# Kernel tuning notes

Hardware: AMD Instinct MI355X
Metric: run time of the kernel (lower is better)

## Reference

```python
import jax, jax.numpy as jnp
import numpy as np
from jax import lax

EPS = 1e-5
K = 20

def _bn_lrelu(h, g, b, m, v):
    # inference-style BatchNorm (channel-last) + LeakyReLU(0.2)
    h = (h - m) * (g * lax.rsqrt(v + EPS)) + b
    return jnp.where(h > 0, h, 0.2 * h)

def _edgeconv(x, W, g, b, m, v):
    # x: (B, N, C) -> (B, N, O)
    xx = jnp.sum(x * x, axis=-1)
    # negative squared pairwise distance: -||xi||^2 - ||xj||^2 + 2 xi.xj
    d = 2.0 * jnp.einsum('bnc,bmc->bnm', x, x) - xx[:, :, None] - xx[:, None, :]
    idx = lax.top_k(d, K)[1]  # (B, N, K) indices of nearest neighbors (incl. self)
    nbr = jax.vmap(lambda xb, ib: xb[ib])(x, idx)  # (B, N, K, C)
    ctr = x[:, :, None, :]
    edge = jnp.concatenate([jnp.broadcast_to(ctr, nbr.shape), nbr - ctr], axis=-1)  # (B,N,K,2C)
    h = jnp.einsum('bnkc,oc->bnko', edge, W)  # 1x1 Conv2d, no bias
    h = _bn_lrelu(h, g, b, m, v)
    return jnp.max(h, axis=2)  # max over K neighbors -> (B, N, O)

def _forward(pts, w1, g1, b1, m1, v1, w2, g2, b2, m2, v2, w3, g3, b3, m3, v3, w4, g4, b4, m4, v4, wg, gg, bg, mg, vg):
    x1 = _edgeconv(pts, w1, g1, b1, m1, v1)   # (B,N,64)
    x2 = _edgeconv(x1, w2, g2, b2, m2, v2)    # (B,N,64)
    x3 = _edgeconv(x2, w3, g3, b3, m3, v3)    # (B,N,128)
    x4 = _edgeconv(x3, w4, g4, b4, m4, v4)    # (B,N,256)
    xcat = jnp.concatenate([x1, x2, x3, x4], axis=-1)  # (B,N,512)
    h = jnp.einsum('bnc,oc->bno', xcat, wg)   # 1x1 Conv1d, no bias
    h = _bn_lrelu(h, gg, bg, mg, vg)
    return jnp.max(h, axis=1)[:, :, None]     # (B, feat_dims, 1)

def setup_inputs():
    key = jax.random.key(0)
    ks = jax.random.split(key, 8)
    B, N = 8, 2048
    def w(k_, o, i):
        return jax.random.normal(k_, (o, i), jnp.float32) / np.float32(np.sqrt(i))
    def bn(k_, c):
        k1, k2, k3, k4 = jax.random.split(k_, 4)
        return (jax.random.uniform(k1, (c,), jnp.float32, 0.5, 1.5),
                jax.random.normal(k2, (c,), jnp.float32) * 0.1,
                jax.random.normal(k3, (c,), jnp.float32) * 0.1,
                jax.random.uniform(k4, (c,), jnp.float32, 0.5, 1.5))
    inp = {'pts': jax.random.normal(ks[0], (B, N, 3), jnp.float32)}
    chans = [(3, 64), (64, 64), (64, 128), (128, 256)]
    for i, (ci, co) in enumerate(chans, start=1):
        inp[f'w{i}'] = w(jax.random.fold_in(ks[1], i), co, 2 * ci)
        g, b, m, v = bn(jax.random.fold_in(ks[2], i), co)
        inp[f'g{i}'], inp[f'b{i}'], inp[f'm{i}'], inp[f'v{i}'] = g, b, m, v
    inp['wg'] = w(ks[3], 512, 512)
    inp['gg'], inp['bg'], inp['mg'], inp['vg'] = bn(ks[4], 512)
    return inp

def reference(pts, w1, g1, b1, m1, v1, w2, g2, b2, m2, v2, w3, g3, b3, m3, v3, w4, g4, b4, m4, v4, wg, gg, bg, mg, vg):
    return _forward(pts, w1, g1, b1, m1, v1, w2, g2, b2, m2, v2, w3, g3, b3, m3, v3, w4, g4, b4, m4, v4, wg, gg, bg, mg, vg)
```

## Files before the change

kernel.cpp:

```cpp
#include <hip/hip_runtime.h>
#include <hip/hip_bf16.h>

#define EPS 1e-5f

typedef __attribute__((ext_vector_type(8))) short bf16x8;
typedef __attribute__((ext_vector_type(4))) float f32x4;

__device__ __forceinline__ unsigned int fkey(float f) {
    unsigned int b = __float_as_uint(f);
    return (b & 0x80000000u) ? ~b : (b | 0x80000000u);
}
__device__ __forceinline__ float funkey(unsigned int k) {
    unsigned int b = (k & 0x80000000u) ? (k & 0x7fffffffu) : ~k;
    return __uint_as_float(b);
}
__device__ __forceinline__ unsigned short f2bu(float f) {
    union { __hip_bfloat16 h; unsigned short u; } cv;
    cv.h = __float2bfloat16(f);
    return cv.u;
}
__device__ __forceinline__ float bu2f(unsigned short u) {
    return __uint_as_float(((unsigned int)u) << 16);
}
__device__ __forceinline__ void hilo(float v, unsigned short& h, unsigned short& l) {
    h = f2bu(v);
    l = f2bu(v - bu2f(h));
}

__global__ void wfrag_kernel(const float* __restrict__ W, int CO, int C2, int C2P,
                             unsigned short* __restrict__ Fh, unsigned short* __restrict__ Fl) {
    int id = blockIdx.x * 256 + threadIdx.x;
    int total = CO * C2P;
    if (id >= total) return;
    int j = id & 7, lane = (id >> 3) & 63, t = id >> 9;
    int KS = C2P >> 5;
    int ks = t % KS, ot = t / KS;
    int o = ot * 16 + (lane & 15);
    int c = ks * 32 + ((lane >> 4) << 3) + j;
    float v = (c < C2) ? W[o * C2 + c] : 0.f;
    unsigned short h, l;
    hilo(v, h, l);
    Fh[id] = h;
    Fl[id] = l;
}

__global__ void xfrag_kernel(const float* __restrict__ feat, int fs, int C, int KS,
                             unsigned short* __restrict__ Fh, unsigned short* __restrict__ Fl) {
    const int N = 2048, NT = 128;
    int id = blockIdx.x * 256 + threadIdx.x;
    int total = 8 * NT * KS * 512;
    if (id >= total) return;
    int j = id & 7, lane = (id >> 3) & 63;
    int rest = id >> 9;
    int ks = rest % KS;
    int bt = rest / KS;
    int t = bt & 127, b = bt >> 7;
    int row = t * 16 + (lane & 15);
    int c = ks * 32 + ((lane >> 4) << 3) + j;
    float v = (c < C) ? feat[((size_t)(b * N + row)) * fs + c] : 0.f;
    unsigned short h, l;
    hilo(v, h, l);
    Fh[id] = h;
    Fl[id] = l;
}

__global__ void sumsq_feat_kernel(const float* __restrict__ feat, int fs, int C,
                                  float* __restrict__ xx) {
    int id = blockIdx.x * 256 + threadIdx.x;
    if (id >= 8 * 2048) return;
    const float* p = feat + (size_t)id * fs;
    float s = 0.f;
    if ((C & 3) == 0) {
        for (int c = 0; c < C; c += 4) {
            float4 v = *(const float4*)(p + c);
            s = fmaf(v.x, v.x, s); s = fmaf(v.y, v.y, s);
            s = fmaf(v.z, v.z, s); s = fmaf(v.w, v.w, s);
        }
    } else {
        for (int c = 0; c < C; ++c) { float v = p[c]; s = fmaf(v, v, s); }
    }
    xx[id] = s;
}

template <int CP>
__global__ __launch_bounds__(512, 4) void
dist_topk_mfma(const unsigned short* __restrict__ Fh, const unsigned short* __restrict__ Fl,
               const float* __restrict__ xx, int* __restrict__ idxOut) {
    const int N = 2048, NT = 128, CAP = 448;
    constexpr int KS = CP / 32;
    int b  = blockIdx.x & 7;
    int mt = blockIdx.x >> 3;
    int tid = threadIdx.x, lane = tid & 63, wv = tid >> 6;

    __shared__ unsigned int gmax[16][64];
    __shared__ unsigned int Tsh[16];
    __shared__ unsigned int cnt[16];
    __shared__ unsigned long long cand[16][CAP];

    bf16x8 Ah[KS], Al[KS];
#pragma unroll
    for (int ks = 0; ks < KS; ++ks) {
        size_t fi = (((size_t)(b * NT + mt) * KS + ks) << 9) + (lane << 3);
        Ah[ks] = *(const bf16x8*)(Fh + fi);
        Al[ks] = *(const bf16x8*)(Fl + fi);
    }
    int rbase = (lane >> 4) << 2;
    float xxr[4];
#pragma unroll
    for (int rr = 0; rr < 4; ++rr) xxr[rr] = xx[b * N + mt * 16 + rbase + rr];

    auto gramkeys = [&](int ct, unsigned int* kout) {
        f32x4 acc;
#pragma unroll
        for (int rr = 0; rr < 4; ++rr) acc[rr] = 0.f;
#pragma unroll
        for (int ks = 0; ks < KS; ++ks) {
            size_t fi = (((size_t)(b * NT + ct) * KS + ks) << 9) + (lane << 3);
            bf16x8 Bh = *(const bf16x8*)(Fh + fi);
            bf16x8 Bl = *(const bf16x8*)(Fl + fi);
            acc = __builtin_amdgcn_mfma_f32_16x16x32_bf16(Al[ks], Bh, acc, 0, 0, 0);
            acc = __builtin_amdgcn_mfma_f32_16x16x32_bf16(Ah[ks], Bl, acc, 0, 0, 0);
            acc = __builtin_amdgcn_mfma_f32_16x16x32_bf16(Ah[ks], Bh, acc, 0, 0, 0);
        }
        float xxm = xx[b * N + ct * 16 + (lane & 15)];
#pragma unroll
        for (int rr = 0; rr < 4; ++rr)
            kout[rr] = fkey(2.f * acc[rr] - xxr[rr] - xxm);
    };

    unsigned int rmax0[4], rmax1[4];
#pragma unroll
    for (int rr = 0; rr < 4; ++rr) { rmax0[rr] = 0u; rmax1[rr] = 0u; }

    for (int i = 0; i < 8; ++i) {
        unsigned int kk[4];
        gramkeys(wv * 16 + i, kk);
#pragma unroll
        for (int rr = 0; rr < 4; ++rr) rmax0[rr] = rmax0[rr] > kk[rr] ? rmax0[rr] : kk[rr];
    }
    for (int i = 8; i < 16; ++i) {
        unsigned int kk[4];
        gramkeys(wv * 16 + i, kk);
#pragma unroll
        for (int rr = 0; rr < 4; ++rr) rmax1[rr] = rmax1[rr] > kk[rr] ? rmax1[rr] : kk[rr];
    }
#pragma unroll
    for (int s = 4; s <= 8; s <<= 1)
#pragma unroll
        for (int rr = 0; rr < 4; ++rr) {
            unsigned int o0 = (unsigned int)__shfl_xor((int)rmax0[rr], s);
            rmax0[rr] = rmax0[rr] > o0 ? rmax0[rr] : o0;
            unsigned int o1 = (unsigned int)__shfl_xor((int)rmax1[rr], s);
            rmax1[rr] = rmax1[rr] > o1 ? rmax1[rr] : o1;
        }
    if ((lane & 15) < 4) {
#pragma unroll
        for (int rr = 0; rr < 4; ++rr) {
            gmax[rbase + rr][wv * 8 + (lane & 3)]     = rmax0[rr];
            gmax[rbase + rr][wv * 8 + 4 + (lane & 3)] = rmax1[rr];
        }
    }
    __syncthreads();

#pragma unroll
    for (int pass = 0; pass < 2; ++pass) {
        int row = wv + 8 * pass;
        unsigned int S = gmax[row][lane];
#pragma unroll
        for (int k = 2; k <= 64; k <<= 1)
#pragma unroll
            for (int j2 = k >> 1; j2 > 0; j2 >>= 1) {
                unsigned int o = (unsigned int)__shfl_xor((int)S, j2);
                bool keepMax = (((lane & j2) == 0) == ((lane & k) == 0));
                unsigned int mx = S > o ? S : o;
                unsigned int mn = S > o ? o : S;
                S = keepMax ? mx : mn;
            }
        if (lane == 19) Tsh[row] = S;
        if (lane == 0) cnt[row] = 0u;
    }
    __syncthreads();

    for (int i = 0; i < 16; ++i) {
        int ct = wv * 16 + i;
        unsigned int kk[4];
        gramkeys(ct, kk);
        int m = ct * 16 + (lane & 15);
#pragma unroll
        for (int rr = 0; rr < 4; ++rr) {
            int row = rbase + rr;
            if (kk[rr] >= Tsh[row]) {
                unsigned int slot = atomicAdd(&cnt[row], 1u);
                if (slot < CAP)
                    cand[row][slot] = ((unsigned long long)kk[rr] << 16) |
                                      (unsigned long long)(0xFFFFu - (unsigned int)m);
            }
        }
    }
    __syncthreads();

#pragma unroll
    for (int pass = 0; pass < 2; ++pass) {
        int row = wv + 8 * pass;
        unsigned int nc = cnt[row];
        if (nc <= 64u) {
            unsigned long long P = (lane < (int)nc) ? cand[row][lane] : 0ULL;
#pragma unroll
            for (int k = 2; k <= 64; k <<= 1)
#pragma unroll
                for (int j2 = k >> 1; j2 > 0; j2 >>= 1) {
                    unsigned long long o = __shfl_xor(P, j2);
                    bool keepMax = (((lane & j2) == 0) == ((lane & k) == 0));
                    unsigned long long mx = P > o ? P : o;
                    unsigned long long mn = P > o ? o : P;
                    P = keepMax ? mx : mn;
                }
            if (lane < 20)
                idxOut[((size_t)b * N + mt * 16 + row) * 20 + lane] =
                    (int)(0xFFFFu - (unsigned int)(P & 0xFFFFu));
        } else {
            unsigned int ncc = nc < CAP ? nc : CAP;
            unsigned long long P0 = ((unsigned int)(lane)       < ncc) ? cand[row][lane]       : 0ULL;
            unsigned long long P1 = ((unsigned int)(lane + 64)  < ncc) ? cand[row][lane + 64]  : 0ULL;
            unsigned long long P2 = ((unsigned int)(lane + 128) < ncc) ? cand[row][lane + 128] : 0ULL;
            unsigned long long P3 = ((unsigned int)(lane + 192) < ncc) ? cand[row][lane + 192] : 0ULL;
            unsigned long long P4 = ((unsigned int)(lane + 256) < ncc) ? cand[row][lane + 256] : 0ULL;
            unsigned long long P5 = ((unsigned int)(lane + 320) < ncc) ? cand[row][lane + 320] : 0ULL;
            unsigned long long P6 = ((unsigned int)(lane + 384) < ncc) ? cand[row][lane + 384] : 0ULL;
            int resm = 0;
            for (int k = 0; k < 20; ++k) {
                unsigned long long lmx = P0;
                lmx = lmx > P1 ? lmx : P1;
                lmx = lmx > P2 ? lmx : P2;
                lmx = lmx > P3 ? lmx : P3;
                lmx = lmx > P4 ? lmx : P4;
                lmx = lmx > P5 ? lmx : P5;
                lmx = lmx > P6 ? lmx : P6;
#pragma unroll
                for (int s = 1; s < 64; s <<= 1) {
                    unsigned long long o = __shfl_xor(lmx, s);
                    lmx = lmx > o ? lmx : o;
                }
                P0 = (P0 == lmx) ? 0ULL : P0;
                P1 = (P1 == lmx) ? 0ULL : P1;
                P2 = (P2 == lmx) ? 0ULL : P2;
                P3 = (P3 == lmx) ? 0ULL : P3;
                P4 = (P4 == lmx) ? 0ULL : P4;
                P5 = (P5 == lmx) ? 0ULL : P5;
                P6 = (P6 == lmx) ? 0ULL : P6;
                if (lane == k) resm = (int)(0xFFFFu - (unsigned int)(lmx & 0xFFFFu));
            }
            if (lane < 20) idxOut[((size_t)b * N + mt * 16 + row) * 20 + lane] = resm;
        }
    }
}

template <int CI, int CO, int TN, int WAVES, int NKC>
__global__ __launch_bounds__(WAVES * 64) void
edgeconv_mfma(const float* __restrict__ feat, int fs, const int* __restrict__ idx,
              const unsigned short* __restrict__ Wh, const unsigned short* __restrict__ Wl,
              const float* __restrict__ gp, const float* __restrict__ bp,
              const float* __restrict__ mp, const float* __restrict__ vp,
              float* __restrict__ outBase) {
    constexpr int N = 2048, K = 20;
    constexpr int C2 = 2 * CI;
    constexpr int C2P = (C2 < 32) ? 32 : C2;
    constexpr int KS = C2P / 32;
    constexpr int KSC = KS / NKC;
    constexpr int CCOLS = KSC * 32;
    constexpr int CHB = CCOLS * 2;
    constexpr int OT = CO / 16;
    constexpr int OTW = OT / WAVES;
    constexpr int M = TN * K;
    constexpr int MT = M / 16;
    constexpr int CH = CCOLS / 8;
    constexpr int SWZ = (CHB >= 128) ? 7 : (CHB / 16 - 1);
    constexpr int THREADS = WAVES * 64;

    int b  = blockIdx.x & 7;
    int n0 = (blockIdx.x >> 3) * TN;
    int tid = threadIdx.x;
    int lane = tid & 63, wv = tid >> 6;

    __shared__ float ctr[TN][CI];
    __shared__ int nb[M];
    __shared__ __align__(16) unsigned char Eh[M * CHB];
    __shared__ __align__(16) unsigned char El[M * CHB];

    for (int e = tid; e < TN * CI; e += THREADS) {
        int ln = e / CI, c = e % CI;
        ctr[ln][c] = feat[((size_t)b * N + n0 + ln) * fs + c];
    }
    for (int e = tid; e < M; e += THREADS) {
        int k = e / TN, ln = e % TN;
        nb[e] = idx[((size_t)b * N + n0 + ln) * K + k];
    }
    __syncthreads();

    f32x4 acc[MT][OTW];
#pragma unroll
    for (int mt = 0; mt < MT; ++mt)
#pragma unroll
        for (int ot = 0; ot < OTW; ++ot)
#pragma unroll
            for (int rr = 0; rr < 4; ++rr) acc[mt][ot][rr] = 0.f;

    for (int kc = 0; kc < NKC; ++kc) {
        if (kc) __syncthreads();
        for (int e = tid; e < M * CH; e += THREADS) {
            int mrow = e / CH, ch = e - mrow * CH;
            int c0 = kc * CCOLS + ch * 8;
            int ln = mrow % TN;
            float v[8];
            if constexpr (CI >= 8) {
                if (c0 < CI) {
#pragma unroll
                    for (int j = 0; j < 8; ++j) v[j] = ctr[ln][c0 + j];
                } else {
                    int c1 = c0 - CI;
                    const float* nrow = feat + ((size_t)b * N + nb[mrow]) * fs + c1;
                    float4 a  = *(const float4*)nrow;
                    float4 b4 = *(const float4*)(nrow + 4);
                    v[0] = a.x  - ctr[ln][c1 + 0];
                    v[1] = a.y  - ctr[ln][c1 + 1];
                    v[2] = a.z  - ctr[ln][c1 + 2];
                    v[3] = a.w  - ctr[ln][c1 + 3];
                    v[4] = b4.x - ctr[ln][c1 + 4];
                    v[5] = b4.y - ctr[ln][c1 + 5];
                    v[6] = b4.z - ctr[ln][c1 + 6];
                    v[7] = b4.w - ctr[ln][c1 + 7];
                }
            } else {
                if (c0 == 0) {
                    const float* nrow = feat + ((size_t)b * N + nb[mrow]) * fs;
                    v[0] = ctr[ln][0]; v[1] = ctr[ln][1]; v[2] = ctr[ln][2];
                    v[3] = nrow[0] - ctr[ln][0];
                    v[4] = nrow[1] - ctr[ln][1];
                    v[5] = nrow[2] - ctr[ln][2];
                    v[6] = 0.f; v[7] = 0.f;
                } else {
#pragma unroll
                    for (int j = 0; j < 8; ++j) v[j] = 0.f;
                }
            }
            union { unsigned short u[8]; uint4 v4; } th, tl;
#pragma unroll
            for (int j = 0; j < 8; ++j) hilo(v[j], th.u[j], tl.u[j]);
            int off = mrow * CHB + ((ch * 16) ^ ((mrow & SWZ) << 4));
            *(uint4*)&Eh[off] = th.v4;
            *(uint4*)&El[off] = tl.v4;
        }
        __syncthreads();

        bf16x8 Bh[OTW][KSC], Bl[OTW][KSC];
#pragma unroll
        for (int ot = 0; ot < OTW; ++ot)
#pragma unroll
            for (int ksc = 0; ksc < KSC; ++ksc) {
                size_t fi = (size_t)((((wv * OTW + ot) * KS + kc * KSC + ksc) * 64 + lane)) << 3;
                Bh[ot][ksc] = *(const bf16x8*)(Wh + fi);
                Bl[ot][ksc] = *(const bf16x8*)(Wl + fi);
            }

#pragma unroll
        for (int mt = 0; mt < MT; ++mt) {
            int r0 = mt * 16 + (lane & 15);
            int cb = (lane >> 4) << 4;
            bf16x8 Ah[KSC], Al[KSC];
#pragma unroll
            for (int ksc = 0; ksc < KSC; ++ksc) {
                int off = r0 * CHB + (((ksc << 6) + cb) ^ ((r0 & SWZ) << 4));
                Ah[ksc] = *(const bf16x8*)&Eh[off];
                Al[ksc] = *(const bf16x8*)&El[off];
            }
#pragma unroll
            for (int ksc = 0; ksc < KSC; ++ksc)
#pragma unroll
                for (int ot = 0; ot < OTW; ++ot) {
                    acc[mt][ot] = __builtin_amdgcn_mfma_f32_16x16x32_bf16(Al[ksc], Bh[ot][ksc], acc[mt][ot], 0, 0, 0);
                    acc[mt][ot] = __builtin_amdgcn_mfma_f32_16x16x32_bf16(Ah[ksc], Bl[ot][ksc], acc[mt][ot], 0, 0, 0);
                    acc[mt][ot] = __builtin_amdgcn_mfma_f32_16x16x32_bf16(Ah[ksc], Bh[ot][ksc], acc[mt][ot], 0, 0, 0);
                }
        }
    }

#pragma unroll
    for (int ot = 0; ot < OTW; ++ot) {
        f32x4 v;
#pragma unroll
        for (int rr = 0; rr < 4; ++rr) {
            float m = acc[0][ot][rr];
#pragma unroll
            for (int mt = 1; mt < MT; ++mt) m = fmaxf(m, acc[mt][ot][rr]);
            if constexpr (TN == 4) m = fmaxf(m, __shfl_xor(m, 16));
            m = fmaxf(m, __shfl_xor(m, 32));
            v[rr] = m;
        }
        int o = (wv * OTW + ot) * 16 + (lane & 15);
        float s  = gp[o] * rsqrtf(vp[o] + EPS);
        float sh = bp[o] - mp[o] * s;
        bool valid = (TN == 8) ? (lane < 32) : (lane < 16);
        if (valid) {
            int lnb = (TN == 8) ? ((lane >> 4) << 2) : 0;
#pragma unroll
            for (int rr = 0; rr < 4; ++rr) {
                float h = fmaf(v[rr], s, sh);
                h = h > 0.f ? h : 0.2f * h;
                outBase[((size_t)b * N + n0 + lnb + rr) * 512 + o] = h;
            }
        }
    }
}

__global__ __launch_bounds__(256) void
global_mfma(const float* __restrict__ xcat,
            const unsigned short* __restrict__ Wh, const unsigned short* __restrict__ Wl,
            const float* __restrict__ gg, const float* __restrict__ bg,
            const float* __restrict__ mg, const float* __restrict__ vg,
            unsigned int* __restrict__ keys) {
    const int N = 2048, CV = 512;
    int b     = blockIdx.x & 7;
    int t     = blockIdx.x >> 3;
    int n0    = (t & 63) * 32;
    int colh  = t >> 6;
    int tid = threadIdx.x, lane = tid & 63, wv = tid >> 6;
    int obase = colh * 16 + wv * 4;

    f32x4 acc0[4], acc1[4];
#pragma unroll
    for (int ot = 0; ot < 4; ++ot)
#pragma unroll
        for (int rr = 0; rr < 4; ++rr) { acc0[ot][rr] = 0.f; acc1[ot][rr] = 0.f; }

    const float* arow0 = xcat + ((size_t)b * N + n0 +      (lane & 15)) * CV + ((lane >> 4) << 3);
    const float* arow1 = xcat + ((size_t)b * N + n0 + 16 + (lane & 15)) * CV + ((lane >> 4) << 3);

    for (int ks = 0; ks < 16; ++ks) {
        bf16x8 Ah0, Al0, Ah1, Al1;
        {
            float4 a  = *(const float4*)(arow0 + ks * 32);
            float4 b4 = *(const float4*)(arow0 + ks * 32 + 4);
            union { unsigned short u[8]; bf16x8 v; } ch, cl;
            hilo(a.x,  ch.u[0], cl.u[0]); hilo(a.y,  ch.u[1], cl.u[1]);
            hilo(a.z,  ch.u[2], cl.u[2]); hilo(a.w,  ch.u[3], cl.u[3]);
            hilo(b4.x, ch.u[4], cl.u[4]); hilo(b4.y, ch.u[5], cl.u[5]);
            hilo(b4.z, ch.u[6], cl.u[6]); hilo(b4.w, ch.u[7], cl.u[7]);
            Ah0 = ch.v; Al0 = cl.v;
        }
        {
            float4 a  = *(const float4*)(arow1 + ks * 32);
            float4 b4 = *(const float4*)(arow1 + ks * 32 + 4);
            union { unsigned short u[8]; bf16x8 v; } ch, cl;
            hilo(a.x,  ch.u[0], cl.u[0]); hilo(a.y,  ch.u[1], cl.u[1]);
            hilo(a.z,  ch.u[2], cl.u[2]); hilo(a.w,  ch.u[3], cl.u[3]);
            hilo(b4.x, ch.u[4], cl.u[4]); hilo(b4.y, ch.u[5], cl.u[5]);
            hilo(b4.z, ch.u[6], cl.u[6]); hilo(b4.w, ch.u[7], cl.u[7]);
            Ah1 = ch.v; Al1 = cl.v;
        }
#pragma unroll
        for (int ot = 0; ot < 4; ++ot) {
            size_t fi = (size_t)((((obase + ot) * 16 + ks) * 64 + lane)) << 3;
            bf16x8 Bh = *(const bf16x8*)(Wh + fi);
            bf16x8 Bl = *(const bf16x8*)(Wl + fi);
            acc0[ot] = __builtin_amdgcn_mfma_f32_16x16x32_bf16(Al0, Bh, acc0[ot], 0, 0, 0);
            acc0[ot] = __builtin_amdgcn_mfma_f32_16x16x32_bf16(Ah0, Bl, acc0[ot], 0, 0, 0);
            acc0[ot] = __builtin_amdgcn_mfma_f32_16x16x32_bf16(Ah0, Bh, acc0[ot], 0, 0, 0);
            acc1[ot] = __builtin_amdgcn_mfma_f32_16x16x32_bf16(Al1, Bh, acc1[ot], 0, 0, 0);
            acc1[ot] = __builtin_amdgcn_mfma_f32_16x16x32_bf16(Ah1, Bl, acc1[ot], 0, 0, 0);
            acc1[ot] = __builtin_amdgcn_mfma_f32_16x16x32_bf16(Ah1, Bh, acc1[ot], 0, 0, 0);
        }
    }

#pragma unroll
    for (int ot = 0; ot < 4; ++ot) {
        f32x4 v;
#pragma unroll
        for (int rr = 0; rr < 4; ++rr) {
            float m = fmaxf(acc0[ot][rr], acc1[ot][rr]);
            m = fmaxf(m, __shfl_xor(m, 16));
            m = fmaxf(m, __shfl_xor(m, 32));
            v[rr] = m;
        }
        int o = (obase + ot) * 16 + (lane & 15);
        float s  = gg[o] * rsqrtf(vg[o] + EPS);
        float sh = bg[o] - mg[o] * s;
        if (lane < 16) {
            float hm = -INFINITY;
#pragma unroll
            for (int rr = 0; rr < 4; ++rr) {
                float h = fmaf(v[rr], s, sh);
                h = h > 0.f ? h : 0.2f * h;
                hm = fmaxf(hm, h);
            }
            atomicMax(&keys[b * 512 + o], fkey(hm));
        }
    }
}

__global__ void decode_kernel(const unsigned int* __restrict__ keys, float* __restrict__ out) {
    int id = blockIdx.x * 256 + threadIdx.x;
    if (id < 8 * 512) out[id] = funkey(keys[id]);
}

extern "C" void kernel_launch(void* const* d_in, const int* in_sizes, int n_in,
                              void* d_out, int out_size, void* d_ws, size_t ws_size,
                              hipStream_t stream) {
    const int B = 8, N = 2048, K = 20;
    const float* pts = (const float*)d_in[0];
    const float* w1 = (const float*)d_in[1];
    const float *g1 = (const float*)d_in[2], *b1 = (const float*)d_in[3],
                *m1 = (const float*)d_in[4], *v1 = (const float*)d_in[5];
    const float* w2 = (const float*)d_in[6];
    const float *g2 = (const float*)d_in[7], *b2 = (const float*)d_in[8],
                *m2 = (const float*)d_in[9], *v2 = (const float*)d_in[10];
    const float* w3 = (const float*)d_in[11];
    const float *g3 = (const float*)d_in[12], *b3 = (const float*)d_in[13],
                *m3 = (const float*)d_in[14], *v3 = (const float*)d_in[15];
    const float* w4 = (const float*)d_in[16];
    const float *g4 = (const float*)d_in[17], *b4 = (const float*)d_in[18],
                *m4 = (const float*)d_in[19], *v4 = (const float*)d_in[20];
    const float* wg = (const float*)d_in[21];
    const float *gg = (const float*)d_in[22], *bg = (const float*)d_in[23],
                *mg = (const float*)d_in[24], *vg = (const float*)d_in[25];

    float* ws   = (float*)d_ws;
    float* xcat = ws;
    float* xx   = xcat + (size_t)B * N * 512;
    int*   idx  = (int*)(xx + B * N);
    unsigned short* Fdh = (unsigned short*)(idx + (size_t)B * N * K);
    unsigned short* Fdl = Fdh + (size_t)B * N * 128;
    unsigned short* wf1h = Fdl + (size_t)B * N * 128;
    unsigned short* wf1l = wf1h + 64 * 32;
    unsigned short* wf2h = wf1l + 64 * 32;
    unsigned short* wf2l = wf2h + 64 * 128;
    unsigned short* wf3h = wf2l + 64 * 128;
    unsigned short* wf3l = wf3h + 128 * 128;
    unsigned short* wf4h = wf3l + 128 * 128;
    unsigned short* wf4l = wf4h + 256 * 256;
    unsigned short* wfgh = wf4l + 256 * 256;
    unsigned short* wfgl = wfgh + 512 * 512;
    unsigned int* keys  = (unsigned int*)(wfgl + 512 * 512);

    wfrag_kernel<<<(64 * 32 + 255) / 256, 256, 0, stream>>>(w1, 64, 6, 32, wf1h, wf1l);
    wfrag_kernel<<<(64 * 128 + 255) / 256, 256, 0, stream>>>(w2, 64, 128, 128, wf2h, wf2l);
    wfrag_kernel<<<(128 * 128 + 255) / 256, 256, 0, stream>>>(w3, 128, 128, 128, wf3h, wf3l);
    wfrag_kernel<<<(256 * 256 + 255) / 256, 256, 0, stream>>>(w4, 256, 256, 256, wf4h, wf4l);
    wfrag_kernel<<<(512 * 512 + 255) / 256, 256, 0, stream>>>(wg, 512, 512, 512, wfgh, wfgl);

    xfrag_kernel<<<(8 * 128 * 1 * 512 + 255) / 256, 256, 0, stream>>>(pts, 3, 3, 1, Fdh, Fdl);
    sumsq_feat_kernel<<<(B * N + 255) / 256, 256, 0, stream>>>(pts, 3, 3, xx);
    dist_topk_mfma<32><<<B * (N / 16), 512, 0, stream>>>(Fdh, Fdl, xx, idx);
    edgeconv_mfma<3, 64, 8, 4, 1><<<B * (N / 8), 256, 0, stream>>>(pts, 3, idx, wf1h, wf1l, g1, b1, m1, v1, xcat + 0);

    xfrag_kernel<<<(8 * 128 * 2 * 512 + 255) / 256, 256, 0, stream>>>(xcat + 0, 512, 64, 2, Fdh, Fdl);
    sumsq_feat_kernel<<<(B * N + 255) / 256, 256, 0, stream>>>(xcat + 0, 512, 64, xx);
    dist_topk_mfma<64><<<B * (N / 16), 512, 0, stream>>>(Fdh, Fdl, xx, idx);
    edgeconv_mfma<64, 64, 4, 4, 1><<<B * (N / 4), 256, 0, stream>>>(xcat + 0, 512, idx, wf2h, wf2l, g2, b2, m2, v2, xcat + 64);

    xfrag_kernel<<<(8 * 128 * 2 * 512 + 255) / 256, 256, 0, stream>>>(xcat + 64, 512, 64, 2, Fdh, Fdl);
    sumsq_feat_kernel<<<(B * N + 255) / 256, 256, 0, stream>>>(xcat + 64, 512, 64, xx);
    dist_topk_mfma<64><<<B * (N / 16), 512, 0, stream>>>(Fdh, Fdl, xx, idx);
    edgeconv_mfma<64, 128, 4, 8, 1><<<B * (N / 4), 512, 0, stream>>>(xcat + 64, 512, idx, wf3h, wf3l, g3, b3, m3, v3, xcat + 128);

    xfrag_kernel<<<(8 * 128 * 4 * 512 + 255) / 256, 256, 0, stream>>>(xcat + 128, 512, 128, 4, Fdh, Fdl);
    sumsq_feat_kernel<<<(B * N + 255) / 256, 256, 0, stream>>>(xcat + 128, 512, 128, xx);
    dist_topk_mfma<128><<<B * (N / 16), 512, 0, stream>>>(Fdh, Fdl, xx, idx);
    edgeconv_mfma<128, 256, 4, 8, 2><<<B * (N / 4), 512, 0, stream>>>(xcat + 128, 512, idx, wf4h, wf4l, g4, b4, m4, v4, xcat + 256);

    hipMemsetAsync(keys, 0, (size_t)B * 512 * sizeof(unsigned int), stream);
    global_mfma<<<B * 128, 256, 0, stream>>>(xcat, wfgh, wfgl, gg, bg, mg, vg, keys);
    decode_kernel<<<(B * 512 + 255) / 256, 256, 0, stream>>>(keys, (float*)d_out);
}
```

Baseline: 506.2 us.

## Split edge conv weights into center and difference parts, precompute center term per point

Splits each EdgeConv weight into a center half and a neighbor-difference half. The center contribution W_c·x_i is computed once per point by a new ctr_mfma kernel that reuses the existing distance fragments, rather than once for each of the K neighbors. The edge kernel then multiplies only the difference features and adds the precomputed center term before BN and LeakyReLU, which halves its GEMM K dimension and its LDS staging and removes the multi-chunk loop. In exchange it adds one kernel launch per layer and a global buffer write and read for the center outputs.

```diff
diff --git a/kernel.cpp b/kernel.cpp
--- a/kernel.cpp
+++ b/kernel.cpp
@@ -27,7 +27,7 @@
     l = f2bu(v - bu2f(h));
 }
 
-__global__ void wfrag_kernel(const float* __restrict__ W, int CO, int C2, int C2P,
+__global__ void wfrag_kernel(const float* __restrict__ W, int CO, int CIN, int coff, int CW, int C2P,
                              unsigned short* __restrict__ Fh, unsigned short* __restrict__ Fl) {
     int id = blockIdx.x * 256 + threadIdx.x;
     int total = CO * C2P;
@@ -37,7 +37,7 @@
     int ks = t % KS, ot = t / KS;
     int o = ot * 16 + (lane & 15);
     int c = ks * 32 + ((lane >> 4) << 3) + j;
-    float v = (c < C2) ? W[o * C2 + c] : 0.f;
+    float v = (c < CW) ? W[o * CIN + coff + c] : 0.f;
     unsigned short h, l;
     hilo(v, h, l);
     Fh[id] = h;
@@ -255,26 +255,71 @@
     }
 }
 
-template <int CI, int CO, int TN, int WAVES, int NKC>
+template <int CP, int CO>
+__global__ __launch_bounds__(256) void
+ctr_mfma(const unsigned short* __restrict__ Fh, const unsigned short* __restrict__ Fl,
+         const unsigned short* __restrict__ Wh, const unsigned short* __restrict__ Wl,
+         float* __restrict__ out) {
+    const int N = 2048, NT = 128;
+    constexpr int KS = CP / 32;
+    constexpr int OTW = CO / 64;
+    int b  = blockIdx.x & 7;
+    int mt = blockIdx.x >> 3;
+    int tid = threadIdx.x, lane = tid & 63, wv = tid >> 6;
+
+    bf16x8 Ah[KS], Al[KS];
+#pragma unroll
+    for (int ks = 0; ks < KS; ++ks) {
+        size_t fi = (((size_t)(b * NT + mt) * KS + ks) << 9) + (lane << 3);
+        Ah[ks] = *(const bf16x8*)(Fh + fi);
+        Al[ks] = *(const bf16x8*)(Fl + fi);
+    }
+    int rbase = (lane >> 4) << 2;
+
+    f32x4 acc[OTW];
+#pragma unroll
+    for (int ot = 0; ot < OTW; ++ot)
+#pragma unroll
+        for (int rr = 0; rr < 4; ++rr) acc[ot][rr] = 0.f;
+
+#pragma unroll
+    for (int ot = 0; ot < OTW; ++ot)
+#pragma unroll
+        for (int ks = 0; ks < KS; ++ks) {
+            size_t fi = (size_t)((((wv * OTW + ot) * KS + ks) * 64 + lane)) << 3;
+            bf16x8 Bh = *(const bf16x8*)(Wh + fi);
+            bf16x8 Bl = *(const bf16x8*)(Wl + fi);
+            acc[ot] = __builtin_amdgcn_mfma_f32_16x16x32_bf16(Al[ks], Bh, acc[ot], 0, 0, 0);
+            acc[ot] = __builtin_amdgcn_mfma_f32_16x16x32_bf16(Ah[ks], Bl, acc[ot], 0, 0, 0);
+            acc[ot] = __builtin_amdgcn_mfma_f32_16x16x32_bf16(Ah[ks], Bh, acc[ot], 0, 0, 0);
+        }
+
+#pragma unroll
+    for (int ot = 0; ot < OTW; ++ot) {
+        int o = (wv * OTW + ot) * 16 + (lane & 15);
+#pragma unroll
+        for (int rr = 0; rr < 4; ++rr)
+            out[((size_t)(b * N + mt * 16 + rbase + rr)) * CO + o] = acc[ot][rr];
+    }
+}
+
+template <int CI, int CP, int CO, int TN, int WAVES>
 __global__ __launch_bounds__(WAVES * 64) void
 edgeconv_mfma(const float* __restrict__ feat, int fs, const int* __restrict__ idx,
               const unsigned short* __restrict__ Wh, const unsigned short* __restrict__ Wl,
+              const float* __restrict__ ctrin,
               const float* __restrict__ gp, const float* __restrict__ bp,
               const float* __restrict__ mp, const float* __restrict__ vp,
               float* __restrict__ outBase) {
     constexpr int N = 2048, K = 20;
-    constexpr int C2 = 2 * CI;
-    constexpr int C2P = (C2 < 32) ? 32 : C2;
-    constexpr int KS = C2P / 32;
-    constexpr int KSC = KS / NKC;
-    constexpr int CCOLS = KSC * 32;
-    constexpr int CHB = CCOLS * 2;
+    constexpr int KS = CP / 32;
+    constexpr int CHB = CP * 2;
+    constexpr int CH = CP / 8;
     constexpr int OT = CO / 16;
     constexpr int OTW = OT / WAVES;
     constexpr int M = TN * K;
     constexpr int MT = M / 16;
-    constexpr int CH = CCOLS / 8;
-    constexpr int SWZ = (CHB >= 128) ? 7 : (CHB / 16 - 1);
+    constexpr int SWZ = (CHB / 16 - 1) > 15 ? 15 : (CHB / 16 - 1);
     constexpr int THREADS = WAVES * 64;
 
     int b  = blockIdx.x & 7;
@@ -297,6 +342,54 @@
     }
     __syncthreads();
 
+    for (int e = tid; e < M * CH; e += THREADS) {
+        int mrow = e / CH, ch = e - mrow * CH;
+        int c0 = ch * 8;
+        int ln = mrow % TN;
+        float v[8];
+        if constexpr (CI >= 8) {
+            const float* nrow = feat + ((size_t)b * N + nb[mrow]) * fs + c0;
+            float4 a  = *(const float4*)nrow;
+            float4 b4 = *(const float4*)(nrow + 4);
+            v[0] = a.x  - ctr[ln][c0 + 0];
+            v[1] = a.y  - ctr[ln][c0 + 1];
+            v[2] = a.z  - ctr[ln][c0 + 2];
+            v[3] = a.w  - ctr[ln][c0 + 3];
+            v[4] = b4.x - ctr[ln][c0 + 4];
+            v[5] = b4.y - ctr[ln][c0 + 5];
+            v[6] = b4.z - ctr[ln][c0 + 6];
+            v[7] = b4.w - ctr[ln][c0 + 7];
+        } else {
+            if (c0 == 0) {
+                const float* nrow = feat + ((size_t)b * N + nb[mrow]) * fs;
+                v[0] = nrow[0] - ctr[ln][0];
+                v[1] = nrow[1] - ctr[ln][1];
+                v[2] = nrow[2] - ctr[ln][2];
+                v[3] = 0.f; v[4] = 0.f; v[5] = 0.f; v[6] = 0.f; v[7] = 0.f;
+            } else {
+#pragma unroll
+                for (int j = 0; j < 8; ++j) v[j] = 0.f;
+            }
+        }
+        union { unsigned short u[8]; uint4 v4; } th, tl;
+#pragma unroll
+        for (int j = 0; j < 8; ++j) hilo(v[j], th.u[j], tl.u[j]);
+        int off = mrow * CHB + ((ch * 16) ^ ((mrow & SWZ) << 4));
+        *(uint4*)&Eh[off] = th.v4;
+        *(uint4*)&El[off] = tl.v4;
+    }
+    __syncthreads();
+
+    bf16x8 Bh[OTW][KS], Bl[OTW][KS];
+#pragma unroll
+    for (int ot = 0; ot < OTW; ++ot)
+#pragma unroll
+        for (int ks = 0; ks < KS; ++ks) {
+            size_t fi = (size_t)((((wv * OTW + ot) * KS + ks) * 64 + lane)) << 3;
+            Bh[ot][ks] = *(const bf16x8*)(Wh + fi);
+            Bl[ot][ks] = *(const bf16x8*)(Wl + fi);
+        }
+
     f32x4 acc[MT][OTW];
 #pragma unroll
     for (int mt = 0; mt < MT; ++mt)
@@ -305,83 +398,25 @@
 #pragma unroll
             for (int rr = 0; rr < 4; ++rr) acc[mt][ot][rr] = 0.f;
 
-    for (int kc = 0; kc < NKC; ++kc) {
-        if (kc) __syncthreads();
-        for (int e = tid; e < M * CH; e += THREADS) {
-            int mrow = e / CH, ch = e - mrow * CH;
-            int c0 = kc * CCOLS + ch * 8;
-            int ln = mrow % TN;
-            float v[8];
-            if constexpr (CI >= 8) {
-                if (c0 < CI) {
-#pragma unroll
-                    for (int j = 0; j < 8; ++j) v[j] = ctr[ln][c0 + j];
-                } else {
-                    int c1 = c0 - CI;
-                    const float* nrow = feat + ((size_t)b * N + nb[mrow]) * fs + c1;
-                    float4 a  = *(const float4*)nrow;
-                    float4 b4 = *(const float4*)(nrow + 4);
-                    v[0] = a.x  - ctr[ln][c1 + 0];
-                    v[1] = a.y  - ctr[ln][c1 + 1];
-                    v[2] = a.z  - ctr[ln][c1 + 2];
-                    v[3] = a.w  - ctr[ln][c1 + 3];
-                    v[4] = b4.x - ctr[ln][c1 + 4];
-                    v[5] = b4.y - ctr[ln][c1 + 5];
-                    v[6] = b4.z - ctr[ln][c1 + 6];
-                    v[7] = b4.w - ctr[ln][c1 + 7];
-                }
-            } else {
-                if (c0 == 0) {
-                    const float* nrow = feat + ((size_t)b * N + nb[mrow]) * fs;
-                    v[0] = ctr[ln][0]; v[1] = ctr[ln][1]; v[2] = ctr[ln][2];
-                    v[3] = nrow[0] - ctr[ln][0];
-                    v[4] = nrow[1] - ctr[ln][1];
-                    v[5] = nrow[2] - ctr[ln][2];
-                    v[6] = 0.f; v[7] = 0.f;
-                } else {
-#pragma unroll
-                    for (int j = 0; j < 8; ++j) v[j] = 0.f;
-                }
+#pragma unroll
+    for (int mt = 0; mt < MT; ++mt) {
+        int r0 = mt * 16 + (lane & 15);
+        int cb = (lane >> 4) << 4;
+        bf16x8 Ah[KS], Al[KS];
+#pragma unroll
+        for (int ks = 0; ks < KS; ++ks) {
+            int off = r0 * CHB + (((ks << 6) + cb) ^ ((r0 & SWZ) << 4));
+            Ah[ks] = *(const bf16x8*)&Eh[off];
+            Al[ks] = *(const bf16x8*)&El[off];
+        }
+#pragma unroll
+        for (int ks = 0; ks < KS; ++ks)
+#pragma unroll
+            for (int ot = 0; ot < OTW; ++ot) {
+                acc[mt][ot] = __builtin_amdgcn_mfma_f32_16x16x32_bf16(Al[ks], Bh[ot][ks], acc[mt][ot], 0, 0, 0);
+                acc[mt][ot] = __builtin_amdgcn_mfma_f32_16x16x32_bf16(Ah[ks], Bl[ot][ks], acc[mt][ot], 0, 0, 0);
+                acc[mt][ot] = __builtin_amdgcn_mfma_f32_16x16x32_bf16(Ah[ks], Bh[ot][ks], acc[mt][ot], 0, 0, 0);
             }
-            union { unsigned short u[8]; uint4 v4; } th, tl;
-#pragma unroll
-            for (int j = 0; j < 8; ++j) hilo(v[j], th.u[j], tl.u[j]);
-            int off = mrow * CHB + ((ch * 16) ^ ((mrow & SWZ) << 4));
-            *(uint4*)&Eh[off] = th.v4;
-            *(uint4*)&El[off] = tl.v4;
-        }
-        __syncthreads();
-
-        bf16x8 Bh[OTW][KSC], Bl[OTW][KSC];
-#pragma unroll
-        for (int ot = 0; ot < OTW; ++ot)
-#pragma unroll
-            for (int ksc = 0; ksc < KSC; ++ksc) {
-                size_t fi = (size_t)((((wv * OTW + ot) * KS + kc * KSC + ksc) * 64 + lane)) << 3;
-                Bh[ot][ksc] = *(const bf16x8*)(Wh + fi);
-                Bl[ot][ksc] = *(const bf16x8*)(Wl + fi);
-            }
-
-#pragma unroll
-        for (int mt = 0; mt < MT; ++mt) {
-            int r0 = mt * 16 + (lane & 15);
-            int cb = (lane >> 4) << 4;
-            bf16x8 Ah[KSC], Al[KSC];
-#pragma unroll
-            for (int ksc = 0; ksc < KSC; ++ksc) {
-                int off = r0 * CHB + (((ksc << 6) + cb) ^ ((r0 & SWZ) << 4));
-                Ah[ksc] = *(const bf16x8*)&Eh[off];
-                Al[ksc] = *(const bf16x8*)&El[off];
-            }
-#pragma unroll
-            for (int ksc = 0; ksc < KSC; ++ksc)
-#pragma unroll
-                for (int ot = 0; ot < OTW; ++ot) {
-                    acc[mt][ot] = __builtin_amdgcn_mfma_f32_16x16x32_bf16(Al[ksc], Bh[ot][ksc], acc[mt][ot], 0, 0, 0);
-                    acc[mt][ot] = __builtin_amdgcn_mfma_f32_16x16x32_bf16(Ah[ksc], Bl[ot][ksc], acc[mt][ot], 0, 0, 0);
-                    acc[mt][ot] = __builtin_amdgcn_mfma_f32_16x16x32_bf16(Ah[ksc], Bh[ot][ksc], acc[mt][ot], 0, 0, 0);
-                }
-        }
     }
 
 #pragma unroll
@@ -404,7 +439,8 @@
             int lnb = (TN == 8) ? ((lane >> 4) << 2) : 0;
 #pragma unroll
             for (int rr = 0; rr < 4; ++rr) {
-                float h = fmaf(v[rr], s, sh);
+                float c = ctrin[((size_t)(b * N + n0 + lnb + rr)) * CO + o];
+                float h = fmaf(v[rr] + c, s, sh);
                 h = h > 0.f ? h : 0.2f * h;
                 outBase[((size_t)b * N + n0 + lnb + rr) * 512 + o] = h;
             }
@@ -526,46 +562,63 @@
     float* ws   = (float*)d_ws;
     float* xcat = ws;
     float* xx   = xcat + (size_t)B * N * 512;
-    int*   idx  = (int*)(xx + B * N);
+    float* ctro = xx + (size_t)B * N;
+    int*   idx  = (int*)(ctro + (size_t)B * N * 256);
     unsigned short* Fdh = (unsigned short*)(idx + (size_t)B * N * K);
     unsigned short* Fdl = Fdh + (size_t)B * N * 128;
-    unsigned short* wf1h = Fdl + (size_t)B * N * 128;
-    unsigned short* wf1l = wf1h + 64 * 32;
-    unsigned short* wf2h = wf1l + 64 * 32;
-    unsigned short* wf2l = wf2h + 64 * 128;
-    unsigned short* wf3h = wf2l + 64 * 128;
-    unsigned short* wf3l = wf3h + 128 * 128;
-    unsigned short* wf4h = wf3l + 128 * 128;
-    unsigned short* wf4l = wf4h + 256 * 256;
-    unsigned short* wfgh = wf4l + 256 * 256;
+    unsigned short* wc1h = Fdl + (size_t)B * N * 128;
+    unsigned short* wc1l = wc1h + 64 * 32;
+    unsigned short* wd1h = wc1l + 64 * 32;
+    unsigned short* wd1l = wd1h + 64 * 32;
+    unsigned short* wc2h = wd1l + 64 * 32;
+    unsigned short* wc2l = wc2h + 64 * 64;
+    unsigned short* wd2h = wc2l + 64 * 64;
+    unsigned short* wd2l = wd2h + 64 * 64;
+    unsigned short* wc3h = wd2l + 64 * 64;
+    unsigned short* wc3l = wc3h + 128 * 64;
+    unsigned short* wd3h = wc3l + 128 * 64;
+    unsigned short* wd3l = wd3h + 128 * 64;
+    unsigned short* wc4h = wd3l + 128 * 64;
+    unsigned short* wc4l = wc4h + 256 * 128;
+    unsigned short* wd4h = wc4l + 256 * 128;
+    unsigned short* wd4l = wd4h + 256 * 128;
+    unsigned short* wfgh = wd4l + 256 * 128;
     unsigned short* wfgl = wfgh + 512 * 512;
     unsigned int* keys  = (unsigned int*)(wfgl + 512 * 512);
 
-    wfrag_kernel<<<(64 * 32 + 255) / 256, 256, 0, stream>>>(w1, 64, 6, 32, wf1h, wf1l);
-    wfrag_kernel<<<(64 * 128 + 255) / 256, 256, 0, stream>>>(w2, 64, 128, 128, wf2h, wf2l);
-    wfrag_kernel<<<(128 * 128 + 255) / 256, 256, 0, stream>>>(w3, 128, 128, 128, wf3h, wf3l);
-    wfrag_kernel<<<(256 * 256 + 255) / 256, 256, 0, stream>>>(w4, 256, 256, 256, wf4h, wf4l);
-    wfrag_kernel<<<(512 * 512 + 255) / 256, 256, 0, stream>>>(wg, 512, 512, 512, wfgh, wfgl);
+    wfrag_kernel<<<(64 * 32 + 255) / 256, 256, 0, stream>>>(w1, 64, 6, 0, 3, 32, wc1h, wc1l);
+    wfrag_kernel<<<(64 * 32 + 255) / 256, 256, 0, stream>>>(w1, 64, 6, 3, 3, 32, wd1h, wd1l);
+    wfrag_kernel<<<(64 * 64 + 255) / 256, 256, 0, stream>>>(w2, 64, 128, 0, 64, 64, wc2h, wc2l);
+    wfrag_kernel<<<(64 * 64 + 255) / 256, 256, 0, stream>>>(w2, 64, 128, 64, 64, 64, wd2h, wd2l);
+    wfrag_kernel<<<(128 * 64 + 255) / 256, 256, 0, stream>>>(w3, 128, 128, 0, 64, 64, wc3h, wc3l);
+    wfrag_kernel<<<(128 * 64 + 255) / 256, 256, 0, stream>>>(w3, 128, 128, 64, 64, 64, wd3h, wd3l);
+    wfrag_kernel<<<(256 * 128 + 255) / 256, 256, 0, stream>>>(w4, 256, 256, 0, 128, 128, wc4h, wc4l);
+    wfrag_kernel<<<(256 * 128 + 255) / 256, 256, 0, stream>>>(w4, 256, 256, 128, 128, 128, wd4h, wd4l);
+    wfrag_kernel<<<(512 * 512 + 255) / 256, 256, 0, stream>>>(wg, 512, 512, 0, 512, 512, wfgh, wfgl);
 
     xfrag_kernel<<<(8 * 128 * 1 * 512 + 255) / 256, 256, 0, stream>>>(pts, 3, 3, 1, Fdh, Fdl);
     sumsq_feat_kernel<<<(B * N + 255) / 256, 256, 0, stream>>>(pts, 3, 3, xx);
     dist_topk_mfma<32><<<B * (N / 16), 512, 0, stream>>>(Fdh, Fdl, xx, idx);
-    edgeconv_mfma<3, 64, 8, 4, 1><<<B * (N / 8), 256, 0, stream>>>(pts, 3, idx, wf1h, wf1l, g1, b1, m1, v1, xcat + 0);
+    ctr_mfma<32, 64><<<B * 128, 256, 0, stream>>>(Fdh, Fdl, wc1h, wc1l, ctro);
+    edgeconv_mfma<3, 32, 64, 8, 4><<<B * (N / 8), 256, 0, stream>>>(pts, 3, idx, wd1h, wd1l, ctro, g1, b1, m1, v1, xcat + 0);
 
     xfrag_kernel<<<(8 * 128 * 2 * 512 + 255) / 256, 256, 0, stream>>>(xcat + 0, 512, 64, 2, Fdh, Fdl);
     sumsq_feat_kernel<<<(B * N + 255) / 256, 256, 0, stream>>>(xcat + 0, 512, 64, xx);
     dist_topk_mfma<64><<<B * (N / 16), 512, 0, stream>>>(Fdh, Fdl, xx, idx);
-    edgeconv_mfma<64, 64, 4, 4, 1><<<B * (N / 4), 256, 0, stream>>>(xcat + 0, 512, idx, wf2h, wf2l, g2, b2, m2, v2, xcat + 64);
+    ctr_mfma<64, 64><<<B * 128, 256, 0, stream>>>(Fdh, Fdl, wc2h, wc2l, ctro);
+    edgeconv_mfma<64, 64, 64, 4, 4><<<B * (N / 4), 256, 0, stream>>>(xcat + 0, 512, idx, wd2h, wd2l, ctro, g2, b2, m2, v2, xcat + 64);
 
     xfrag_kernel<<<(8 * 128 * 2 * 512 + 255) / 256, 256, 0, stream>>>(xcat + 64, 512, 64, 2, Fdh, Fdl);
     sumsq_feat_kernel<<<(B * N + 255) / 256, 256, 0, stream>>>(xcat + 64, 512, 64, xx);
     dist_topk_mfma<64><<<B * (N / 16), 512, 0, stream>>>(Fdh, Fdl, xx, idx);
-    edgeconv_mfma<64, 128, 4, 8, 1><<<B * (N / 4), 512, 0, stream>>>(xcat + 64, 512, idx, wf3h, wf3l, g3, b3, m3, v3, xcat + 128);
+    ctr_mfma<64, 128><<<B * 128, 256, 0, stream>>>(Fdh, Fdl, wc3h, wc3l, ctro);
+    edgeconv_mfma<64, 64, 128, 4, 8><<<B * (N / 4), 512, 0, stream>>>(xcat + 64, 512, idx, wd3h, wd3l, ctro, g3, b3, m3, v3, xcat + 128);
 
     xfrag_kernel<<<(8 * 128 * 4 * 512 + 255) / 256, 256, 0, stream>>>(xcat + 128, 512, 128, 4, Fdh, Fdl);
     sumsq_feat_kernel<<<(B * N + 255) / 256, 256, 0, stream>>>(xcat + 128, 512, 128, xx);
     dist_topk_mfma<128><<<B * (N / 16), 512, 0, stream>>>(Fdh, Fdl, xx, idx);
-    edgeconv_mfma<128, 256, 4, 8, 2><<<B * (N / 4), 512, 0, stream>>>(xcat + 128, 512, idx, wf4h, wf4l, g4, b4, m4, v4, xcat + 256);
+    ctr_mfma<128, 256><<<B * 128, 256, 0, stream>>>(Fdh, Fdl, wc4h, wc4l, ctro);
+    edgeconv_mfma<128, 128, 256, 4, 8><<<B * (N / 4), 512, 0, stream>>>(xcat + 128, 512, idx, wd4h, wd4l, ctro, g4, b4, m4, v4, xcat + 256);
 
     hipMemsetAsync(keys, 0, (size_t)B * 512 * sizeof(unsigned int), stream);
     global_mfma<<<B * 128, 256, 0, stream>>>(xcat, wfgh, wfgl, gg, bg, mg, vg, keys);
```

Result: faster. 469.9 us (-7.2%).
